# Kernel tuning notes

Hardware: AMD Instinct MI355X
Metric: run time of the kernel (lower is better)

Reference implementation:

```python
import jax, jax.numpy as jnp
import numpy as np

NUM_EMB = 1024
EMB_DIM = 64


def setup_inputs() -> dict:
    key = jax.random.key(0)
    k1, k2 = jax.random.split(key)
    x = jax.random.normal(k1, (32, EMB_DIM, 4096), dtype=jnp.float32)
    # nn.Embedding weight initialized uniform(-1/K, 1/K)
    emb = jax.random.uniform(k2, (NUM_EMB, EMB_DIM), dtype=jnp.float32,
                             minval=-1.0 / NUM_EMB, maxval=1.0 / NUM_EMB)
    return {"x": x, "emb": emb}


def reference(x, emb):
    D = emb.shape[1]
    # Faithful to torch .view(-1, D): raw row-major flatten of contiguous x
    xf = x.reshape(-1, D)                                   # [N, D]
    # ||xf||^2 + ||e||^2 - 2 xf e^T  (cdist^2 via matmul)
    d = (jnp.sum(xf * xf, axis=1, keepdims=True)
         + jnp.sum(emb * emb, axis=1)
         - 2.0 * xf @ emb.T)                                # [N, K]
    idx = jnp.argmin(d, axis=1)                             # [N] int
    idx = idx.reshape((x.shape[0],) + x.shape[2:])          # [B, T]
    quantized = emb[idx].reshape(x.shape)                   # raw reshape, as view_as
    return quantized, idx
```

## Files before the change

kernel.cpp:

```cpp
#include <hip/hip_runtime.h>


#define N_ROWS   131072
#define NUM_EMB  1024
#define EMB_DIM  64
#define Q_ELEMS  8388608
#define THREADS  512
#define ROWS_PB  128
#define KCHUNK   128
#define NCHUNKS  8
#define WCAP     1024

typedef short short8 __attribute__((ext_vector_type(8)));
typedef float f32x4  __attribute__((ext_vector_type(4)));

__device__ __forceinline__ unsigned short bf16_rne(float f) {
    unsigned u = __float_as_uint(f);
    u += 0x7fffu + ((u >> 16) & 1u);
    return (unsigned short)(u >> 16);
}

__device__ __forceinline__ unsigned fkey(float d) {
    unsigned b = __float_as_uint(d);
    return b ^ (((unsigned)((int)b >> 31)) | 0x80000000u);
}

__device__ __forceinline__ float np_sq64(const float* a) {
    #pragma clang fp contract(off)
    float r0=a[0]*a[0],r1=a[1]*a[1],r2=a[2]*a[2],r3=a[3]*a[3];
    float r4=a[4]*a[4],r5=a[5]*a[5],r6=a[6]*a[6],r7=a[7]*a[7];
    #pragma unroll
    for (int i=8;i<64;i+=8){
        r0+=a[i+0]*a[i+0];r1+=a[i+1]*a[i+1];r2+=a[i+2]*a[i+2];r3+=a[i+3]*a[i+3];
        r4+=a[i+4]*a[i+4];r5+=a[i+5]*a[i+5];r6+=a[i+6]*a[i+6];r7+=a[i+7]*a[i+7];
    }
    return ((r0+r1)+(r2+r3))+((r4+r5)+(r6+r7));
}

__device__ __forceinline__ float rotmin16(float v) {
    int x;
    x = __builtin_amdgcn_update_dpp(0, __float_as_int(v), 0x121, 0xf, 0xf, true);
    v = fminf(v, __int_as_float(x));
    x = __builtin_amdgcn_update_dpp(0, __float_as_int(v), 0x122, 0xf, 0xf, true);
    v = fminf(v, __int_as_float(x));
    x = __builtin_amdgcn_update_dpp(0, __float_as_int(v), 0x124, 0xf, 0xf, true);
    v = fminf(v, __int_as_float(x));
    x = __builtin_amdgcn_update_dpp(0, __float_as_int(v), 0x128, 0xf, 0xf, true);
    v = fminf(v, __int_as_float(x));
    return v;
}

__global__ __launch_bounds__(256) void vq_prep(const float* __restrict__ emb,
                                               float* __restrict__ sume,
                                               unsigned short* __restrict__ ehg) {
    int k = blockIdx.x * 256 + threadIdx.x;
    if (k < NUM_EMB) {
        sume[k] = np_sq64(emb + (k << 6));
        int c = k >> 7, krow = k & 127;
        #pragma unroll
        for (int gp = 0; gp < 8; ++gp) {
            short8 h;
            #pragma unroll
            for (int j = 0; j < 8; ++j)
                h[j] = (short)bf16_rne(emb[(k << 6) + gp*8 + j]);
            reinterpret_cast<short8*>(ehg)[c*1024 + gp*128 + krow] = h;
        }
    }
}

__global__ __launch_bounds__(THREADS, 8)
void vq_main(const float* __restrict__ x, const float* __restrict__ emb,
             const float* __restrict__ sume_g, const unsigned short* __restrict__ ehg,
             float* __restrict__ out_q, float* __restrict__ out_idx) {
    __shared__ int4     EH4[1024];
    __shared__ float    SUME[NUM_EMB];
    __shared__ float    RMIN[ROWS_PB];
    __shared__ float    THR[ROWS_PB];
    __shared__ float    SA[ROWS_PB];
    __shared__ int      WL[WCAP];
    __shared__ unsigned DMIN[ROWS_PB];
    __shared__ unsigned KMIN[ROWS_PB];
    __shared__ int      SIDX[ROWS_PB];
    __shared__ unsigned WCNT;

    const int t   = threadIdx.x;
    const int w   = t >> 6;
    const int l   = t & 63;
    const int g   = l >> 4;
    const int c16 = l & 15;
    const size_t blk_row0 = (size_t)blockIdx.x * ROWS_PB;

    const int4* eg4 = reinterpret_cast<const int4*>(ehg);
    int4 sa = eg4[t], sb = eg4[t + 512];

    SUME[t]       = sume_g[t];
    SUME[t + 512] = sume_g[t + 512];
    if (t < ROWS_PB) { DMIN[t] = 0xFFFFFFFFu; KMIN[t] = 0xFFFFFFFFu; }
    if (t == 0) WCNT = 0u;

    short8 ah[2];
    {
        const float* xp = x + (blk_row0 + (size_t)(w*16 + c16)) * EMB_DIM;
        float sabs = 0.f;
        #pragma unroll
        for (int hf = 0; hf < 2; ++hf) {
            #pragma unroll
            for (int j = 0; j < 8; ++j) {
                float v = 2.0f * xp[hf*32 + g*8 + j];
                sabs += fabsf(v);
                ah[hf][j] = (short)bf16_rne(v);
            }
        }
        sabs += __shfl_xor(sabs, 16);
        sabs += __shfl_xor(sabs, 32);
        if (g == 0) SA[w*16 + c16] = sabs;
    }

    float stash[4] = {3.4e38f, 3.4e38f, 3.4e38f, 3.4e38f};

    for (int c = 0; c < NCHUNKS; ++c) {
        EH4[t] = sa; EH4[t + 512] = sb;
        __syncthreads();
        if (c + 1 < NCHUNKS) {
            sa = eg4[(c+1)*1024 + t]; sb = eg4[(c+1)*1024 + t + 512];
        }
        #pragma unroll
        for (int lt = 0; lt < 8; ++lt) {
            const int krow = lt*16 + c16;
            short8 bh0 = reinterpret_cast<const short8*>(EH4)[(g    )*128 + krow];
            short8 bh1 = reinterpret_cast<const short8*>(EH4)[(g + 4)*128 + krow];
            float scol = SUME[c*KCHUNK + krow];
            f32x4 a0 = {0.f,0.f,0.f,0.f};
            a0 = __builtin_amdgcn_mfma_f32_16x16x32_bf16(ah[0], bh0, a0, 0,0,0);
            a0 = __builtin_amdgcn_mfma_f32_16x16x32_bf16(ah[1], bh1, a0, 0,0,0);
            #pragma unroll
            for (int r = 0; r < 4; ++r)
                stash[r] = fminf(stash[r], scol - a0[r]);
        }
        __syncthreads();
    }

    #pragma unroll
    for (int r = 0; r < 4; ++r) {
        float v = rotmin16(stash[r]);
        if (c16 == 0) RMIN[w*16 + 4*g + r] = v;
    }
    __syncthreads();
    if (t < ROWS_PB) {
        THR[t] = RMIN[t] + (SA[t] * 1.6e-5f + 4.0e-5f);
    }
    __syncthreads();
    float thrv[4];
    #pragma unroll
    for (int r = 0; r < 4; ++r) thrv[r] = THR[w*16 + 4*g + r];

    sa = eg4[t]; sb = eg4[t + 512];
    for (int c = 0; c < NCHUNKS; ++c) {
        EH4[t] = sa; EH4[t + 512] = sb;
        __syncthreads();
        if (c + 1 < NCHUNKS) {
            sa = eg4[(c+1)*1024 + t]; sb = eg4[(c+1)*1024 + t + 512];
        }
        #pragma unroll
        for (int lt = 0; lt < 8; ++lt) {
            const int krow = lt*16 + c16;
            short8 bh0 = reinterpret_cast<const short8*>(EH4)[(g    )*128 + krow];
            short8 bh1 = reinterpret_cast<const short8*>(EH4)[(g + 4)*128 + krow];
            float scol = SUME[c*KCHUNK + krow];
            f32x4 a0 = {0.f,0.f,0.f,0.f};
            a0 = __builtin_amdgcn_mfma_f32_16x16x32_bf16(ah[0], bh0, a0, 0,0,0);
            a0 = __builtin_amdgcn_mfma_f32_16x16x32_bf16(ah[1], bh1, a0, 0,0,0);
            const int kk = c*KCHUNK + krow;
            #pragma unroll
            for (int r = 0; r < 4; ++r) {
                float sv = scol - a0[r];
                if (sv < thrv[r]) {
                    unsigned q = atomicAdd(&WCNT, 1u);
                    if (q < WCAP) WL[q] = ((w*16 + 4*g + r) << 10) | kk;
                }
            }
        }
        __syncthreads();
    }

    const unsigned wc = WCNT;
    float* WLD = reinterpret_cast<float*>(EH4);

    if (wc <= WCAP) {
        for (unsigned q = t; q < wc; q += THREADS) {
            int pr = WL[q]; int row = pr >> 10; int kk = pr & 1023;
            const float* xr = x + (blk_row0 + (size_t)row) * EMB_DIM;
            const float* er = emb + (kk << 6);
            float sumx = np_sq64(xr);
            float cc = 0.f;
            #pragma unroll 8
            for (int i = 0; i < EMB_DIM; ++i)
                cc = fmaf(2.0f * xr[i], er[i], cc);
            float d;
            {
                #pragma clang fp contract(off)
                d = (sumx + SUME[kk]) - cc;
            }
            WLD[q] = d;
            atomicMin(&DMIN[row], fkey(d));
        }
        __syncthreads();
        for (unsigned q = t; q < wc; q += THREADS) {
            int pr = WL[q]; int row = pr >> 10; int kk = pr & 1023;
            if (fkey(WLD[q]) == DMIN[row])
                atomicMin(&KMIN[row], (unsigned)kk);
        }
        __syncthreads();
        if (t < ROWS_PB) {
            int bk = (int)KMIN[t];
            SIDX[t] = bk;
            out_idx[blk_row0 + t] = (float)bk;
        }
    } else {
        if (t < ROWS_PB) {
            const float* xr = x + (blk_row0 + (size_t)t) * EMB_DIM;
            float sumx = np_sq64(xr);
            volatile const float* xv = xr;
            float bm = 3.4e38f; int bb = 0;
            for (int kk = 0; kk < NUM_EMB; ++kk) {
                const float* er = emb + (kk << 6);
                float cc = 0.f;
                for (int i = 0; i < EMB_DIM; ++i)
                    cc = fmaf(2.0f * xv[i], er[i], cc);
                {
                    #pragma clang fp contract(off)
                    float d = (sumx + SUME[kk]) - cc;
                    if (d < bm) { bm = d; bb = kk; }
                }
            }
            SIDX[t] = bb;
            out_idx[blk_row0 + t] = (float)bb;
        }
    }
    __syncthreads();

    const float4* emb4 = reinterpret_cast<const float4*>(emb);
    float4* q4 = reinterpret_cast<float4*>(out_q + blk_row0 * EMB_DIM);
    #pragma unroll
    for (int i = 0; i < 4; ++i) {
        int e4 = t + i * THREADS;
        int rr = e4 >> 4, cc2 = e4 & 15;
        q4[e4] = emb4[SIDX[rr]*16 + cc2];
    }
}

extern "C" void kernel_launch(void* const* d_in, const int* in_sizes, int n_in,
                              void* d_out, int out_size, void* d_ws, size_t ws_size,
                              hipStream_t stream) {
    const float* x   = (const float*)d_in[0];
    const float* emb = (const float*)d_in[1];
    float* out_q   = (float*)d_out;
    float* out_idx = out_q + Q_ELEMS;
    float*          sume = (float*)d_ws;
    unsigned short* ehg  = (unsigned short*)((char*)d_ws + 4096);

    vq_prep<<<dim3(NUM_EMB / 256), dim3(256), 0, stream>>>(emb, sume, ehg);
    vq_main<<<dim3(N_ROWS / ROWS_PB), dim3(THREADS), 0, stream>>>(x, emb, sume, ehg,
                                                                  out_q, out_idx);
}
```

Before: 83.17 us.

## Keep codebook slices in registers per wave and share row tiles across waves

Each wave now holds a fixed 128-entry slice of the bf16 codebook and its norms in registers. Every wave computes all 64 rows of the block, and per-wave minima are reduced through shared memory. This removes the per-chunk LDS staging of the codebook and its block barriers, and halves rows per block, which doubles the grid and the global codebook reads. The candidate pass adds a 4-wide early-out test before the per-element atomics, and the launch-bounds occupancy hint drops from 8 to 2, raising register pressure.

```diff
diff --git a/kernel.cpp b/kernel.cpp
--- a/kernel.cpp
+++ b/kernel.cpp
@@ -6,9 +6,8 @@
 #define EMB_DIM  64
 #define Q_ELEMS  8388608
 #define THREADS  512
-#define ROWS_PB  128
-#define KCHUNK   128
-#define NCHUNKS  8
+#define ROWS_PB  64
+#define KSEG     128
 #define WCAP     1024
 
 typedef short short8 __attribute__((ext_vector_type(8)));
@@ -68,16 +67,15 @@
     }
 }
 
-__global__ __launch_bounds__(THREADS, 8)
+__global__ __launch_bounds__(THREADS, 2)
 void vq_main(const float* __restrict__ x, const float* __restrict__ emb,
              const float* __restrict__ sume_g, const unsigned short* __restrict__ ehg,
              float* __restrict__ out_q, float* __restrict__ out_idx) {
-    __shared__ int4     EH4[1024];
-    __shared__ float    SUME[NUM_EMB];
-    __shared__ float    RMIN[ROWS_PB];
+    __shared__ float    LM[8][ROWS_PB];
+    __shared__ float    SA[ROWS_PB];
     __shared__ float    THR[ROWS_PB];
-    __shared__ float    SA[ROWS_PB];
     __shared__ int      WL[WCAP];
+    __shared__ float    WLD[WCAP];
     __shared__ unsigned DMIN[ROWS_PB];
     __shared__ unsigned KMIN[ROWS_PB];
     __shared__ int      SIDX[ROWS_PB];
@@ -90,101 +88,110 @@
     const int c16 = l & 15;
     const size_t blk_row0 = (size_t)blockIdx.x * ROWS_PB;
 
-    const int4* eg4 = reinterpret_cast<const int4*>(ehg);
-    int4 sa = eg4[t], sb = eg4[t + 512];
-
-    SUME[t]       = sume_g[t];
-    SUME[t + 512] = sume_g[t + 512];
+    const short8* eg8 = reinterpret_cast<const short8*>(ehg);
+    short8 eh[8][2];
+    #pragma unroll
+    for (int lt = 0; lt < 8; ++lt) {
+        eh[lt][0] = eg8[w*1024 + (g    )*128 + lt*16 + c16];
+        eh[lt][1] = eg8[w*1024 + (g + 4)*128 + lt*16 + c16];
+    }
+    float smv[8];
+    #pragma unroll
+    for (int lt = 0; lt < 8; ++lt) smv[lt] = sume_g[w*KSEG + lt*16 + c16];
+
     if (t < ROWS_PB) { DMIN[t] = 0xFFFFFFFFu; KMIN[t] = 0xFFFFFFFFu; }
     if (t == 0) WCNT = 0u;
 
-    short8 ah[2];
-    {
-        const float* xp = x + (blk_row0 + (size_t)(w*16 + c16)) * EMB_DIM;
+    short8 ah[4][2];
+    #pragma unroll
+    for (int st = 0; st < 4; ++st) {
+        const float* xp = x + (blk_row0 + (size_t)(st*16 + c16)) * EMB_DIM;
+        const float4* xq = reinterpret_cast<const float4*>(xp);
         float sabs = 0.f;
         #pragma unroll
         for (int hf = 0; hf < 2; ++hf) {
+            float4 u0 = xq[hf*8 + g*2 + 0];
+            float4 u1 = xq[hf*8 + g*2 + 1];
+            float vv[8] = {u0.x,u0.y,u0.z,u0.w,u1.x,u1.y,u1.z,u1.w};
             #pragma unroll
             for (int j = 0; j < 8; ++j) {
-                float v = 2.0f * xp[hf*32 + g*8 + j];
+                float v = 2.0f * vv[j];
                 sabs += fabsf(v);
-                ah[hf][j] = (short)bf16_rne(v);
+                ah[st][hf][j] = (short)bf16_rne(v);
             }
         }
         sabs += __shfl_xor(sabs, 16);
         sabs += __shfl_xor(sabs, 32);
-        if (g == 0) SA[w*16 + c16] = sabs;
-    }
-
-    float stash[4] = {3.4e38f, 3.4e38f, 3.4e38f, 3.4e38f};
-
-    for (int c = 0; c < NCHUNKS; ++c) {
-        EH4[t] = sa; EH4[t + 512] = sb;
-        __syncthreads();
-        if (c + 1 < NCHUNKS) {
-            sa = eg4[(c+1)*1024 + t]; sb = eg4[(c+1)*1024 + t + 512];
-        }
-        #pragma unroll
-        for (int lt = 0; lt < 8; ++lt) {
-            const int krow = lt*16 + c16;
-            short8 bh0 = reinterpret_cast<const short8*>(EH4)[(g    )*128 + krow];
-            short8 bh1 = reinterpret_cast<const short8*>(EH4)[(g + 4)*128 + krow];
-            float scol = SUME[c*KCHUNK + krow];
-            f32x4 a0 = {0.f,0.f,0.f,0.f};
-            a0 = __builtin_amdgcn_mfma_f32_16x16x32_bf16(ah[0], bh0, a0, 0,0,0);
-            a0 = __builtin_amdgcn_mfma_f32_16x16x32_bf16(ah[1], bh1, a0, 0,0,0);
+        if (w == 0 && g == 0) SA[st*16 + c16] = sabs;
+    }
+
+    float stash[4][4];
+    #pragma unroll
+    for (int st = 0; st < 4; ++st)
+        #pragma unroll
+        for (int r = 0; r < 4; ++r) stash[st][r] = 3.4e38f;
+
+    #pragma unroll
+    for (int lt = 0; lt < 8; ++lt) {
+        #pragma unroll
+        for (int st = 0; st < 4; ++st) {
+            f32x4 a = {0.f,0.f,0.f,0.f};
+            a = __builtin_amdgcn_mfma_f32_16x16x32_bf16(ah[st][0], eh[lt][0], a, 0,0,0);
+            a = __builtin_amdgcn_mfma_f32_16x16x32_bf16(ah[st][1], eh[lt][1], a, 0,0,0);
             #pragma unroll
             for (int r = 0; r < 4; ++r)
-                stash[r] = fminf(stash[r], scol - a0[r]);
-        }
-        __syncthreads();
-    }
-
-    #pragma unroll
-    for (int r = 0; r < 4; ++r) {
-        float v = rotmin16(stash[r]);
-        if (c16 == 0) RMIN[w*16 + 4*g + r] = v;
+                stash[st][r] = fminf(stash[st][r], smv[lt] - a[r]);
+        }
+    }
+
+    #pragma unroll
+    for (int st = 0; st < 4; ++st) {
+        #pragma unroll
+        for (int r = 0; r < 4; ++r) {
+            float v = rotmin16(stash[st][r]);
+            if (c16 == 0) LM[w][st*16 + 4*g + r] = v;
+        }
     }
     __syncthreads();
     if (t < ROWS_PB) {
-        THR[t] = RMIN[t] + (SA[t] * 1.6e-5f + 4.0e-5f);
-    }
-    __syncthreads();
-    float thrv[4];
-    #pragma unroll
-    for (int r = 0; r < 4; ++r) thrv[r] = THR[w*16 + 4*g + r];
-
-    sa = eg4[t]; sb = eg4[t + 512];
-    for (int c = 0; c < NCHUNKS; ++c) {
-        EH4[t] = sa; EH4[t + 512] = sb;
-        __syncthreads();
-        if (c + 1 < NCHUNKS) {
-            sa = eg4[(c+1)*1024 + t]; sb = eg4[(c+1)*1024 + t + 512];
-        }
-        #pragma unroll
-        for (int lt = 0; lt < 8; ++lt) {
-            const int krow = lt*16 + c16;
-            short8 bh0 = reinterpret_cast<const short8*>(EH4)[(g    )*128 + krow];
-            short8 bh1 = reinterpret_cast<const short8*>(EH4)[(g + 4)*128 + krow];
-            float scol = SUME[c*KCHUNK + krow];
-            f32x4 a0 = {0.f,0.f,0.f,0.f};
-            a0 = __builtin_amdgcn_mfma_f32_16x16x32_bf16(ah[0], bh0, a0, 0,0,0);
-            a0 = __builtin_amdgcn_mfma_f32_16x16x32_bf16(ah[1], bh1, a0, 0,0,0);
-            const int kk = c*KCHUNK + krow;
-            #pragma unroll
-            for (int r = 0; r < 4; ++r) {
-                float sv = scol - a0[r];
-                if (sv < thrv[r]) {
-                    unsigned q = atomicAdd(&WCNT, 1u);
-                    if (q < WCAP) WL[q] = ((w*16 + 4*g + r) << 10) | kk;
-                }
-            }
-        }
-        __syncthreads();
-    }
+        float bm = LM[0][t];
+        #pragma unroll
+        for (int w2 = 1; w2 < 8; ++w2) bm = fminf(bm, LM[w2][t]);
+        THR[t] = bm + (SA[t] * 1.6e-5f + 4.0e-5f);
+    }
+    __syncthreads();
+
+    float thrv[4][4], thrmax[4];
+    #pragma unroll
+    for (int st = 0; st < 4; ++st) {
+        #pragma unroll
+        for (int r = 0; r < 4; ++r) thrv[st][r] = THR[st*16 + 4*g + r];
+        thrmax[st] = fmaxf(fmaxf(thrv[st][0], thrv[st][1]),
+                           fmaxf(thrv[st][2], thrv[st][3]));
+    }
+
+    #pragma unroll
+    for (int lt = 0; lt < 8; ++lt) {
+        const int kk = w*KSEG + lt*16 + c16;
+        #pragma unroll
+        for (int st = 0; st < 4; ++st) {
+            f32x4 a = {0.f,0.f,0.f,0.f};
+            a = __builtin_amdgcn_mfma_f32_16x16x32_bf16(ah[st][0], eh[lt][0], a, 0,0,0);
+            a = __builtin_amdgcn_mfma_f32_16x16x32_bf16(ah[st][1], eh[lt][1], a, 0,0,0);
+            float s0 = smv[lt] - a[0], s1 = smv[lt] - a[1];
+            float s2 = smv[lt] - a[2], s3 = smv[lt] - a[3];
+            float m4 = fminf(fminf(s0, s1), fminf(s2, s3));
+            if (m4 < thrmax[st]) {
+                if (s0 < thrv[st][0]) { unsigned q = atomicAdd(&WCNT,1u); if (q<WCAP) WL[q] = ((st*16+4*g+0)<<10)|kk; }
+                if (s1 < thrv[st][1]) { unsigned q = atomicAdd(&WCNT,1u); if (q<WCAP) WL[q] = ((st*16+4*g+1)<<10)|kk; }
+                if (s2 < thrv[st][2]) { unsigned q = atomicAdd(&WCNT,1u); if (q<WCAP) WL[q] = ((st*16+4*g+2)<<10)|kk; }
+                if (s3 < thrv[st][3]) { unsigned q = atomicAdd(&WCNT,1u); if (q<WCAP) WL[q] = ((st*16+4*g+3)<<10)|kk; }
+            }
+        }
+    }
+    __syncthreads();
 
     const unsigned wc = WCNT;
-    float* WLD = reinterpret_cast<float*>(EH4);
 
     if (wc <= WCAP) {
         for (unsigned q = t; q < wc; q += THREADS) {
@@ -199,7 +206,7 @@
             float d;
             {
                 #pragma clang fp contract(off)
-                d = (sumx + SUME[kk]) - cc;
+                d = (sumx + sume_g[kk]) - cc;
             }
             WLD[q] = d;
             atomicMin(&DMIN[row], fkey(d));
@@ -229,7 +236,7 @@
                     cc = fmaf(2.0f * xv[i], er[i], cc);
                 {
                     #pragma clang fp contract(off)
-                    float d = (sumx + SUME[kk]) - cc;
+                    float d = (sumx + sume_g[kk]) - cc;
                     if (d < bm) { bm = d; bb = kk; }
                 }
             }
@@ -242,7 +249,7 @@
     const float4* emb4 = reinterpret_cast<const float4*>(emb);
     float4* q4 = reinterpret_cast<float4*>(out_q + blk_row0 * EMB_DIM);
     #pragma unroll
-    for (int i = 0; i < 4; ++i) {
+    for (int i = 0; i < 2; ++i) {
         int e4 = t + i * THREADS;
         int rr = e4 >> 4, cc2 = e4 & 15;
         q4[e4] = emb4[SIDX[rr]*16 + cc2];
```

Result: slower. 148.1 us (+78.0%).
